# Performance work log

Hardware: AMD Instinct MI355X
Metric: run time of the kernel (lower is better)

## Reference

```python
import jax, jax.numpy as jnp
import numpy as np

B, T, D, H = 512, 128, 128, 2048  # batch, seq_len, input/output dim, hidden dim
W_SCALE = 0.02


def setup_inputs() -> dict:
    key = jax.random.key(0)
    ks = jax.random.split(key, 4)
    return {
        "tgt": jax.random.normal(ks[0], (B, T, D), jnp.float32),
        "W_ih": jax.random.normal(ks[1], (4 * H, D), jnp.float32) * W_SCALE,
        "W_hh": jax.random.normal(ks[2], (4 * H, H), jnp.float32) * W_SCALE,
        "b_ih": jnp.zeros((4 * H,), jnp.float32),
        "b_hh": jnp.zeros((4 * H,), jnp.float32),
        "W_out": jax.random.normal(ks[3], (D, H), jnp.float32) * W_SCALE,
        "b_out": jnp.zeros((D,), jnp.float32),
    }


def reference(tgt, W_ih, W_hh, b_ih, b_hh, W_out, b_out):
    # LSTMDecoder.forward with teacher_forcing_ratio=0.0 (deterministic,
    # tgt: [B, T, D]; first frame tgt[:, 0] seeds the decoder.
    batch, max_len, _ = tgt.shape
    hidden = W_hh.shape[1]
    b = b_ih + b_hh  # fuse the two LSTM biases

    def step(carry, _):
        x, h, c = carry
        # torch nn.LSTM gate order: i, f, g, o
        gates = x @ W_ih.T + h @ W_hh.T + b  # [B, 4H]
        i, f, g, o = jnp.split(gates, 4, axis=-1)
        c = jax.nn.sigmoid(f) * c + jax.nn.sigmoid(i) * jnp.tanh(g)
        h = jax.nn.sigmoid(o) * jnp.tanh(c)
        out = h @ W_out.T + b_out  # [B, D]
        return (out, h, c), out

    h0 = jnp.zeros((batch, hidden), tgt.dtype)
    c0 = jnp.zeros((batch, hidden), tgt.dtype)
    _, outs = jax.lax.scan(step, (tgt[:, 0, :], h0, c0), None, length=max_len)
    return outs.transpose(1, 0, 2)  # [B, T, D]
```

## Files before the change

### kernel.cpp

```cpp
#include <hip/hip_runtime.h>
#include <hip/hip_fp16.h>

typedef _Float16 f16;
typedef __attribute__((ext_vector_type(8))) _Float16 f16x8;
typedef __attribute__((ext_vector_type(16))) float f32x16;

#define GLL(src, dst) __builtin_amdgcn_global_load_lds( \
    (const __attribute__((address_space(1))) void*)(src), \
    (__attribute__((address_space(3))) void*)(dst), 16, 0, 0)

__device__ __forceinline__ void gemm_core(
    const f16* __restrict__ A, int lda,
    const f16* __restrict__ Bm, int ldb,
    int K, int bm0, int nbase, int nstride,
    unsigned char* __restrict__ smem, f32x16 acc[2][2])
{
    const int tid  = threadIdx.x;
    const int wave = tid >> 6;
    const int wr   = wave >> 1;
    const int wc   = wave & 1;
    const int lane = tid & 63;
    const int l31  = lane & 31;
    const int hi   = lane >> 5;

    #pragma unroll
    for (int mt = 0; mt < 2; ++mt)
      #pragma unroll
      for (int nt = 0; nt < 2; ++nt)
        #pragma unroll
        for (int e = 0; e < 16; ++e)
          acc[mt][nt][e] = 0.f;

    const f16* gA[4]; const f16* gB[4];
    int ldA[4], ldB[4];
    #pragma unroll
    for (int p = 0; p < 4; ++p) {
        int s  = p * 256 + tid;
        int r  = s >> 3;
        int cg = (s & 7) ^ (r & 7);
        gA[p] = A + (size_t)(bm0 + r) * lda + cg * 8;
        int brow = nbase + (r >> 5) * nstride + (r & 31);
        gB[p] = Bm + (size_t)brow * ldb + cg * 8;
        ldA[p] = (p * 256 + wave * 64) * 16;
        ldB[p] = 16384 + (p * 256 + wave * 64) * 16;
    }

    int offA[2][4], offB[2][4];
    #pragma unroll
    for (int mt = 0; mt < 2; ++mt) {
        int ra = wr * 64 + mt * 32 + l31;
        #pragma unroll
        for (int kk = 0; kk < 4; ++kk)
            offA[mt][kk] = (ra * 8 + ((kk * 2 + hi) ^ (ra & 7))) * 8;
    }
    #pragma unroll
    for (int nt = 0; nt < 2; ++nt) {
        int rb = wc * 64 + nt * 32 + l31;
        #pragma unroll
        for (int kk = 0; kk < 4; ++kk)
            offB[nt][kk] = 8192 + (rb * 8 + ((kk * 2 + hi) ^ (rb & 7))) * 8;
    }

    auto stage = [&](int buf, int t2) {
        unsigned char* base = smem + buf * 32768;
        const int k0 = t2 * 64;
        #pragma unroll
        for (int p = 0; p < 4; ++p) GLL(gA[p] + k0, base + ldA[p]);
        #pragma unroll
        for (int p = 0; p < 4; ++p) GLL(gB[p] + k0, base + ldB[p]);
    };
    auto rdfr = [&](int buf, f16x8 (&af)[2][4], f16x8 (&bf)[2][4]) {
        const f16* base = (const f16*)(smem + buf * 32768);
        #pragma unroll
        for (int mt = 0; mt < 2; ++mt)
          #pragma unroll
          for (int kk = 0; kk < 4; ++kk)
            af[mt][kk] = *(const f16x8*)(base + offA[mt][kk]);
        #pragma unroll
        for (int nt = 0; nt < 2; ++nt)
          #pragma unroll
          for (int kk = 0; kk < 4; ++kk)
            bf[nt][kk] = *(const f16x8*)(base + offB[nt][kk]);
    };
    auto mm = [&](f16x8 (&af)[2][4], f16x8 (&bf)[2][4]) {
        #pragma unroll
        for (int kk = 0; kk < 4; ++kk)
          #pragma unroll
          for (int mt = 0; mt < 2; ++mt)
            #pragma unroll
            for (int nt = 0; nt < 2; ++nt)
              acc[mt][nt] = __builtin_amdgcn_mfma_f32_32x32x16_f16(
                  af[mt][kk], bf[nt][kk], acc[mt][nt], 0, 0, 0);
    };

    const int niter = K >> 6;
    f16x8 aX[2][4], bX[2][4], aY[2][4], bY[2][4];
    stage(0, 0);
    stage(1, 1);
    asm volatile("s_waitcnt vmcnt(8)" ::: "memory");
    __builtin_amdgcn_s_barrier();
    __builtin_amdgcn_sched_barrier(0);
    rdfr(0, aX, bX);

    for (int t = 0; t < niter; t += 2) {
        asm volatile("s_waitcnt lgkmcnt(0)" ::: "memory");
        __builtin_amdgcn_sched_barrier(0);
        __builtin_amdgcn_s_barrier();
        __builtin_amdgcn_sched_barrier(0);
        if (t + 2 < niter) stage(0, t + 2);
        if (t + 2 < niter) asm volatile("s_waitcnt vmcnt(8)" ::: "memory");
        else               asm volatile("s_waitcnt vmcnt(0)" ::: "memory");
        __builtin_amdgcn_s_barrier();
        __builtin_amdgcn_sched_barrier(0);
        rdfr(1, aY, bY);
        mm(aX, bX);
        asm volatile("s_waitcnt lgkmcnt(0)" ::: "memory");
        __builtin_amdgcn_sched_barrier(0);
        __builtin_amdgcn_s_barrier();
        __builtin_amdgcn_sched_barrier(0);
        if (t + 3 < niter) stage(1, t + 3);
        if (t + 2 < niter) {
            if (t + 3 < niter) asm volatile("s_waitcnt vmcnt(8)" ::: "memory");
            else               asm volatile("s_waitcnt vmcnt(0)" ::: "memory");
            __builtin_amdgcn_s_barrier();
            __builtin_amdgcn_sched_barrier(0);
            rdfr(0, aX, bX);
        }
        mm(aY, bY);
    }
}

__global__ __launch_bounds__(256, 1) void k_step(
    const f16* __restrict__ A, int lda, int K,
    const f16* __restrict__ W, int ldb,
    const float* __restrict__ bias,
    float* __restrict__ Cst,
    f16* __restrict__ Hout)
{
    __shared__ alignas(16) unsigned char smem[65536];
    const int hid0 = blockIdx.x * 32;
    const int bm0  = blockIdx.y * 128;
    f32x16 acc[2][2];
    gemm_core(A, lda, W, ldb, K, bm0, hid0, 2048, smem, acc);

    const int tid = threadIdx.x;
    const int wave = tid >> 6, wr = wave >> 1, wc = wave & 1;
    const int lane = tid & 63, l31 = lane & 31, hi = lane >> 5;
    float* G = (float*)smem;
    #pragma unroll
    for (int mt = 0; mt < 2; ++mt)
      #pragma unroll
      for (int nt = 0; nt < 2; ++nt) {
        const int col = wc * 64 + nt * 32 + l31;
        #pragma unroll
        for (int reg = 0; reg < 16; ++reg) {
          const int row = wr * 64 + mt * 32 + (reg & 3) + 8 * (reg >> 2) + 4 * hi;
          G[row * 128 + col] = acc[mt][nt][reg];
        }
      }
    __syncthreads();
    const int hl  = tid & 31;
    const int r8  = tid >> 5;
    const int hid = hid0 + hl;
    const float bI = bias[hid];
    const float bF = bias[2048 + hid];
    const float bG = bias[4096 + hid];
    const float bO = bias[6144 + hid];
    #pragma unroll
    for (int j = 0; j < 16; ++j) {
        const int row = j * 8 + r8;
        const float* g = G + row * 128;
        float iv = g[hl]      + bI;
        float fv = g[32 + hl] + bF;
        float gv = g[64 + hl] + bG;
        float ov = g[96 + hl] + bO;
        float si = 1.f / (1.f + __expf(-iv));
        float sf = 1.f / (1.f + __expf(-fv));
        float so = 1.f / (1.f + __expf(-ov));
        float tg = tanhf(gv);
        const size_t idx = (size_t)(bm0 + row) * 2048 + hid;
        float c = sf * Cst[idx] + si * tg;
        Cst[idx] = c;
        Hout[idx] = (f16)(so * tanhf(c));
    }
}

__global__ __launch_bounds__(256, 1) void k_out(
    const f16* __restrict__ Hbase,
    const f16* __restrict__ Wout,
    const float* __restrict__ bout,
    float* __restrict__ out, int t0)
{
    __shared__ alignas(16) unsigned char smem[65536];
    const int bm0 = blockIdx.y * 128;
    f32x16 acc[2][2];
    gemm_core(Hbase, 2048, Wout, 2048, 2048, bm0, 0, 32, smem, acc);
    const int tid = threadIdx.x;
    const int wave = tid >> 6, wr = wave >> 1, wc = wave & 1;
    const int lane = tid & 63, l31 = lane & 31, hi = lane >> 5;
    #pragma unroll
    for (int mt = 0; mt < 2; ++mt)
      #pragma unroll
      for (int nt = 0; nt < 2; ++nt) {
        const int d = wc * 64 + nt * 32 + l31;
        const float bo = bout[d];
        #pragma unroll
        for (int reg = 0; reg < 16; ++reg) {
          const int row = wr * 64 + mt * 32 + (reg & 3) + 8 * (reg >> 2) + 4 * hi;
          const int m = bm0 + row;
          const int slot = m >> 9, b = m & 511;
          out[(size_t)b * 16384 + (t0 + slot) * 128 + d] = acc[mt][nt][reg] + bo;
        }
      }
}


__global__ void k_cast(const float* __restrict__ s, f16* __restrict__ d, int n)
{
    int i = blockIdx.x * 256 + threadIdx.x;
    if (i < n) d[i] = (f16)s[i];
}

__global__ void k_x0(const float* __restrict__ tgt, f16* __restrict__ x0)
{
    int i = blockIdx.x * 256 + threadIdx.x;
    int b = i >> 7, d = i & 127;
    x0[i] = (f16)tgt[(size_t)b * 16384 + d];
}

__global__ void k_bias(const float* __restrict__ bih, const float* __restrict__ bhh,
                       const float* __restrict__ Wih, const float* __restrict__ bout,
                       float* __restrict__ b0, float* __restrict__ bp)
{
    int r = blockIdx.x * 256 + threadIdx.x;
    if (r >= 8192) return;
    float s = bih[r] + bhh[r];
    float a = 0.f;
    for (int d = 0; d < 128; ++d) a += Wih[(size_t)r * 128 + d] * bout[d];
    b0[r] = s;
    bp[r] = s + a;
}

__global__ void k_wt(const float* __restrict__ Wout, f16* __restrict__ WoutT)
{
    __shared__ float tile[64][65];
    const int k0 = blockIdx.x * 64;
    const int d0 = blockIdx.y * 64;
    const int tid = threadIdx.x;
    const int c = tid & 63, rr = tid >> 6;
    #pragma unroll
    for (int i = 0; i < 16; ++i) {
        int d = rr + i * 4;
        tile[d][c] = Wout[(size_t)(d0 + d) * 2048 + k0 + c];
    }
    __syncthreads();
    #pragma unroll
    for (int i = 0; i < 16; ++i) {
        int k = rr + i * 4;
        WoutT[(size_t)(k0 + k) * 128 + d0 + c] = (f16)tile[c][k];
    }
}

__global__ __launch_bounds__(256, 1) void k_wcomb2(
    const f16* __restrict__ Wih16, const f16* __restrict__ WoutT,
    const float* __restrict__ Whh, f16* __restrict__ Wc)
{
    __shared__ alignas(16) unsigned char smem[65536];
    const int n0  = blockIdx.x * 128;
    const int bm0 = blockIdx.y * 128;
    f32x16 acc[2][2];
    gemm_core(Wih16, 128, WoutT, 128, 128, bm0, n0, 32, smem, acc);
    const int tid = threadIdx.x;
    const int wave = tid >> 6, wr = wave >> 1, wc = wave & 1;
    const int lane = tid & 63, l31 = lane & 31, hi = lane >> 5;
    #pragma unroll
    for (int mt = 0; mt < 2; ++mt)
      #pragma unroll
      for (int nt = 0; nt < 2; ++nt) {
        const int k = n0 + wc * 64 + nt * 32 + l31;
        #pragma unroll
        for (int reg = 0; reg < 16; ++reg) {
          const int row = wr * 64 + mt * 32 + (reg & 3) + 8 * (reg >> 2) + 4 * hi;
          const size_t r = (size_t)(bm0 + row);
          Wc[r * 2048 + k] = (f16)(acc[mt][nt][reg] + Whh[r * 2048 + k]);
        }
      }
}


extern "C" void kernel_launch(void* const* d_in, const int* in_sizes, int n_in,
                              void* d_out, int out_size, void* d_ws, size_t ws_size,
                              hipStream_t stream)
{
    const float* tgt  = (const float*)d_in[0];
    const float* Wih  = (const float*)d_in[1];
    const float* Whh  = (const float*)d_in[2];
    const float* bih  = (const float*)d_in[3];
    const float* bhh  = (const float*)d_in[4];
    const float* Wout = (const float*)d_in[5];
    const float* bout = (const float*)d_in[6];
    float* out = (float*)d_out;

    char* ws = (char*)d_ws;
    size_t off = 0;
    auto alloc = [&](size_t bytes) -> void* {
        void* p = ws + off;
        off += (bytes + 255) & ~(size_t)255;
        return p;
    };
    f16*   Wc     = (f16*)alloc((size_t)8192 * 2048 * 2);
    f16*   Wih16  = (f16*)alloc((size_t)8192 * 128 * 2);
    f16*   Wout16 = (f16*)alloc((size_t)128 * 2048 * 2);
    f16*   WoutT  = (f16*)alloc((size_t)2048 * 128 * 2);
    f16*   x0     = (f16*)alloc((size_t)512 * 128 * 2);
    float* b0     = (float*)alloc(8192 * 4);
    float* bp     = (float*)alloc(8192 * 4);
    float* Cst    = (float*)alloc((size_t)512 * 2048 * 4);

    const size_t slotsz = (size_t)512 * 2048;
    int depth = 0;
    const int cands[7] = {128, 64, 32, 16, 8, 4, 2};
    for (int i = 0; i < 7; ++i)
        if (off + (size_t)cands[i] * slotsz * 2 <= ws_size) { depth = cands[i]; break; }
    if (depth == 0) return;
    f16* Hbuf = (f16*)alloc((size_t)depth * slotsz * 2);

    hipMemsetAsync(Cst, 0, (size_t)512 * 2048 * 4, stream);
    k_cast<<<dim3(4096), dim3(256), 0, stream>>>(Wih, Wih16, 1048576);
    k_cast<<<dim3(1024), dim3(256), 0, stream>>>(Wout, Wout16, 262144);
    k_wt<<<dim3(32, 2), dim3(256), 0, stream>>>(Wout, WoutT);
    k_x0<<<dim3(256), dim3(256), 0, stream>>>(tgt, x0);
    k_bias<<<dim3(32), dim3(256), 0, stream>>>(bih, bhh, Wih, bout, b0, bp);
    k_wcomb2<<<dim3(16, 64), dim3(256), 0, stream>>>(Wih16, WoutT, Whh, Wc);

    k_step<<<dim3(64, 4), dim3(256), 0, stream>>>(x0, 128, 128, Wih16, 128, b0, Cst, Hbuf);
    for (int s = 1; s < 128; ++s) {
        if ((s % depth) == 0)
            k_out<<<dim3(1, depth * 4), dim3(256), 0, stream>>>(Hbuf, Wout16, bout, out, s - depth);
        k_step<<<dim3(64, 4), dim3(256), 0, stream>>>(
            Hbuf + (size_t)((s - 1) % depth) * slotsz, 2048, 2048, Wc, 2048, bp,
            Cst, Hbuf + (size_t)(s % depth) * slotsz);
    }
    k_out<<<dim3(1, depth * 4), dim3(256), 0, stream>>>(Hbuf, Wout16, bout, out, 128 - depth);
}
```

Baseline: 4.307 ms.

## Split GEMM tile across eight waves with simpler single-buffer-read pipeline

```diff
diff --git a/kernel.cpp b/kernel.cpp
--- a/kernel.cpp
+++ b/kernel.cpp
@@ -13,12 +13,12 @@
     const f16* __restrict__ A, int lda,
     const f16* __restrict__ Bm, int ldb,
     int K, int bm0, int nbase, int nstride,
-    unsigned char* __restrict__ smem, f32x16 acc[2][2])
+    unsigned char* __restrict__ smem, f32x16 acc[2])
 {
     const int tid  = threadIdx.x;
     const int wave = tid >> 6;
-    const int wr   = wave >> 1;
-    const int wc   = wave & 1;
+    const int wr   = wave >> 2;
+    const int wc   = wave & 3;
     const int lane = tid & 63;
     const int l31  = lane & 31;
     const int hi   = lane >> 5;
@@ -26,26 +26,24 @@
     #pragma unroll
     for (int mt = 0; mt < 2; ++mt)
       #pragma unroll
-      for (int nt = 0; nt < 2; ++nt)
-        #pragma unroll
-        for (int e = 0; e < 16; ++e)
-          acc[mt][nt][e] = 0.f;
-
-    const f16* gA[4]; const f16* gB[4];
-    int ldA[4], ldB[4];
-    #pragma unroll
-    for (int p = 0; p < 4; ++p) {
-        int s  = p * 256 + tid;
+      for (int e = 0; e < 16; ++e)
+        acc[mt][e] = 0.f;
+
+    const f16* gA[2]; const f16* gB[2];
+    int ldA[2], ldB[2];
+    #pragma unroll
+    for (int p = 0; p < 2; ++p) {
+        int s  = p * 512 + tid;
         int r  = s >> 3;
         int cg = (s & 7) ^ (r & 7);
         gA[p] = A + (size_t)(bm0 + r) * lda + cg * 8;
         int brow = nbase + (r >> 5) * nstride + (r & 31);
         gB[p] = Bm + (size_t)brow * ldb + cg * 8;
-        ldA[p] = (p * 256 + wave * 64) * 16;
-        ldB[p] = 16384 + (p * 256 + wave * 64) * 16;
-    }
-
-    int offA[2][4], offB[2][4];
+        ldA[p] = (p * 512 + wave * 64) * 16;
+        ldB[p] = 16384 + (p * 512 + wave * 64) * 16;
+    }
+
+    int offA[2][4], offB[4];
     #pragma unroll
     for (int mt = 0; mt < 2; ++mt) {
         int ra = wr * 64 + mt * 32 + l31;
@@ -53,84 +51,55 @@
         for (int kk = 0; kk < 4; ++kk)
             offA[mt][kk] = (ra * 8 + ((kk * 2 + hi) ^ (ra & 7))) * 8;
     }
-    #pragma unroll
-    for (int nt = 0; nt < 2; ++nt) {
-        int rb = wc * 64 + nt * 32 + l31;
+    {
+        int rb = wc * 32 + l31;
         #pragma unroll
         for (int kk = 0; kk < 4; ++kk)
-            offB[nt][kk] = 8192 + (rb * 8 + ((kk * 2 + hi) ^ (rb & 7))) * 8;
+            offB[kk] = 8192 + (rb * 8 + ((kk * 2 + hi) ^ (rb & 7))) * 8;
     }
 
     auto stage = [&](int buf, int t2) {
         unsigned char* base = smem + buf * 32768;
         const int k0 = t2 * 64;
         #pragma unroll
-        for (int p = 0; p < 4; ++p) GLL(gA[p] + k0, base + ldA[p]);
-        #pragma unroll
-        for (int p = 0; p < 4; ++p) GLL(gB[p] + k0, base + ldB[p]);
+        for (int p = 0; p < 2; ++p) GLL(gA[p] + k0, base + ldA[p]);
+        #pragma unroll
+        for (int p = 0; p < 2; ++p) GLL(gB[p] + k0, base + ldB[p]);
     };
-    auto rdfr = [&](int buf, f16x8 (&af)[2][4], f16x8 (&bf)[2][4]) {
-        const f16* base = (const f16*)(smem + buf * 32768);
+
+    const int niter = K >> 6;
+    stage(0, 0);
+    stage(1, 1);
+    for (int t = 0; t < niter; ++t) {
+        if (t + 1 < niter)
+            asm volatile("s_waitcnt vmcnt(4)" ::: "memory");
+        else
+            asm volatile("s_waitcnt vmcnt(0)" ::: "memory");
+        __builtin_amdgcn_s_barrier();
+        const f16* base = (const f16*)(smem + (t & 1) * 32768);
+        f16x8 af[2][4], bf[4];
         #pragma unroll
         for (int mt = 0; mt < 2; ++mt)
           #pragma unroll
           for (int kk = 0; kk < 4; ++kk)
             af[mt][kk] = *(const f16x8*)(base + offA[mt][kk]);
         #pragma unroll
-        for (int nt = 0; nt < 2; ++nt)
-          #pragma unroll
-          for (int kk = 0; kk < 4; ++kk)
-            bf[nt][kk] = *(const f16x8*)(base + offB[nt][kk]);
-    };
-    auto mm = [&](f16x8 (&af)[2][4], f16x8 (&bf)[2][4]) {
+        for (int kk = 0; kk < 4; ++kk)
+            bf[kk] = *(const f16x8*)(base + offB[kk]);
+        asm volatile("s_waitcnt lgkmcnt(0)" ::: "memory");
+        __builtin_amdgcn_sched_barrier(0);
+        __builtin_amdgcn_s_barrier();
+        if (t + 2 < niter) stage(t & 1, t + 2);
         #pragma unroll
         for (int kk = 0; kk < 4; ++kk)
           #pragma unroll
           for (int mt = 0; mt < 2; ++mt)
-            #pragma unroll
-            for (int nt = 0; nt < 2; ++nt)
-              acc[mt][nt] = __builtin_amdgcn_mfma_f32_32x32x16_f16(
-                  af[mt][kk], bf[nt][kk], acc[mt][nt], 0, 0, 0);
-    };
-
-    const int niter = K >> 6;
-    f16x8 aX[2][4], bX[2][4], aY[2][4], bY[2][4];
-    stage(0, 0);
-    stage(1, 1);
-    asm volatile("s_waitcnt vmcnt(8)" ::: "memory");
-    __builtin_amdgcn_s_barrier();
-    __builtin_amdgcn_sched_barrier(0);
-    rdfr(0, aX, bX);
-
-    for (int t = 0; t < niter; t += 2) {
-        asm volatile("s_waitcnt lgkmcnt(0)" ::: "memory");
-        __builtin_amdgcn_sched_barrier(0);
-        __builtin_amdgcn_s_barrier();
-        __builtin_amdgcn_sched_barrier(0);
-        if (t + 2 < niter) stage(0, t + 2);
-        if (t + 2 < niter) asm volatile("s_waitcnt vmcnt(8)" ::: "memory");
-        else               asm volatile("s_waitcnt vmcnt(0)" ::: "memory");
-        __builtin_amdgcn_s_barrier();
-        __builtin_amdgcn_sched_barrier(0);
-        rdfr(1, aY, bY);
-        mm(aX, bX);
-        asm volatile("s_waitcnt lgkmcnt(0)" ::: "memory");
-        __builtin_amdgcn_sched_barrier(0);
-        __builtin_amdgcn_s_barrier();
-        __builtin_amdgcn_sched_barrier(0);
-        if (t + 3 < niter) stage(1, t + 3);
-        if (t + 2 < niter) {
-            if (t + 3 < niter) asm volatile("s_waitcnt vmcnt(8)" ::: "memory");
-            else               asm volatile("s_waitcnt vmcnt(0)" ::: "memory");
-            __builtin_amdgcn_s_barrier();
-            __builtin_amdgcn_sched_barrier(0);
-            rdfr(0, aX, bX);
-        }
-        mm(aY, bY);
-    }
-}
-
-__global__ __launch_bounds__(256, 1) void k_step(
+            acc[mt] = __builtin_amdgcn_mfma_f32_32x32x16_f16(
+                af[mt][kk], bf[kk], acc[mt], 0, 0, 0);
+    }
+}
+
+__global__ __launch_bounds__(512, 2) void k_step(
     const f16* __restrict__ A, int lda, int K,
     const f16* __restrict__ W, int ldb,
     const float* __restrict__ bias,
@@ -140,35 +109,33 @@
     __shared__ alignas(16) unsigned char smem[65536];
     const int hid0 = blockIdx.x * 32;
     const int bm0  = blockIdx.y * 128;
-    f32x16 acc[2][2];
+    f32x16 acc[2];
     gemm_core(A, lda, W, ldb, K, bm0, hid0, 2048, smem, acc);
 
     const int tid = threadIdx.x;
-    const int wave = tid >> 6, wr = wave >> 1, wc = wave & 1;
+    const int wave = tid >> 6, wr = wave >> 2, wc = wave & 3;
     const int lane = tid & 63, l31 = lane & 31, hi = lane >> 5;
     float* G = (float*)smem;
     #pragma unroll
-    for (int mt = 0; mt < 2; ++mt)
-      #pragma unroll
-      for (int nt = 0; nt < 2; ++nt) {
-        const int col = wc * 64 + nt * 32 + l31;
+    for (int mt = 0; mt < 2; ++mt) {
+        const int col = wc * 32 + l31;
         #pragma unroll
         for (int reg = 0; reg < 16; ++reg) {
-          const int row = wr * 64 + mt * 32 + (reg & 3) + 8 * (reg >> 2) + 4 * hi;
-          G[row * 128 + col] = acc[mt][nt][reg];
+            const int row = wr * 64 + mt * 32 + (reg & 3) + 8 * (reg >> 2) + 4 * hi;
+            G[row * 128 + col] = acc[mt][reg];
         }
-      }
+    }
     __syncthreads();
     const int hl  = tid & 31;
-    const int r8  = tid >> 5;
+    const int r16 = tid >> 5;
     const int hid = hid0 + hl;
     const float bI = bias[hid];
     const float bF = bias[2048 + hid];
     const float bG = bias[4096 + hid];
     const float bO = bias[6144 + hid];
     #pragma unroll
-    for (int j = 0; j < 16; ++j) {
-        const int row = j * 8 + r8;
+    for (int j = 0; j < 8; ++j) {
+        const int row = j * 16 + r16;
         const float* g = G + row * 128;
         float iv = g[hl]      + bI;
         float fv = g[32 + hl] + bF;
@@ -185,7 +152,7 @@
     }
 }
 
-__global__ __launch_bounds__(256, 1) void k_out(
+__global__ __launch_bounds__(512, 2) void k_out(
     const f16* __restrict__ Hbase,
     const f16* __restrict__ Wout,
     const float* __restrict__ bout,
@@ -193,25 +160,23 @@
 {
     __shared__ alignas(16) unsigned char smem[65536];
     const int bm0 = blockIdx.y * 128;
-    f32x16 acc[2][2];
+    f32x16 acc[2];
     gemm_core(Hbase, 2048, Wout, 2048, 2048, bm0, 0, 32, smem, acc);
     const int tid = threadIdx.x;
-    const int wave = tid >> 6, wr = wave >> 1, wc = wave & 1;
+    const int wave = tid >> 6, wr = wave >> 2, wc = wave & 3;
     const int lane = tid & 63, l31 = lane & 31, hi = lane >> 5;
-    #pragma unroll
-    for (int mt = 0; mt < 2; ++mt)
-      #pragma unroll
-      for (int nt = 0; nt < 2; ++nt) {
-        const int d = wc * 64 + nt * 32 + l31;
-        const float bo = bout[d];
+    const int d = wc * 32 + l31;
+    const float bo = bout[d];
+    #pragma unroll
+    for (int mt = 0; mt < 2; ++mt) {
         #pragma unroll
         for (int reg = 0; reg < 16; ++reg) {
-          const int row = wr * 64 + mt * 32 + (reg & 3) + 8 * (reg >> 2) + 4 * hi;
-          const int m = bm0 + row;
-          const int slot = m >> 9, b = m & 511;
-          out[(size_t)b * 16384 + (t0 + slot) * 128 + d] = acc[mt][nt][reg] + bo;
+            const int row = wr * 64 + mt * 32 + (reg & 3) + 8 * (reg >> 2) + 4 * hi;
+            const int m = bm0 + row;
+            const int slot = m >> 9, b = m & 511;
+            out[(size_t)b * 16384 + (t0 + slot) * 128 + d] = acc[mt][reg] + bo;
         }
-      }
+    }
 }
 
 
@@ -261,30 +226,28 @@
     }
 }
 
-__global__ __launch_bounds__(256, 1) void k_wcomb2(
+__global__ __launch_bounds__(512, 2) void k_wcomb2(
     const f16* __restrict__ Wih16, const f16* __restrict__ WoutT,
     const float* __restrict__ Whh, f16* __restrict__ Wc)
 {
     __shared__ alignas(16) unsigned char smem[65536];
     const int n0  = blockIdx.x * 128;
     const int bm0 = blockIdx.y * 128;
-    f32x16 acc[2][2];
+    f32x16 acc[2];
     gemm_core(Wih16, 128, WoutT, 128, 128, bm0, n0, 32, smem, acc);
     const int tid = threadIdx.x;
-    const int wave = tid >> 6, wr = wave >> 1, wc = wave & 1;
+    const int wave = tid >> 6, wr = wave >> 2, wc = wave & 3;
     const int lane = tid & 63, l31 = lane & 31, hi = lane >> 5;
-    #pragma unroll
-    for (int mt = 0; mt < 2; ++mt)
-      #pragma unroll
-      for (int nt = 0; nt < 2; ++nt) {
-        const int k = n0 + wc * 64 + nt * 32 + l31;
+    const int k = n0 + wc * 32 + l31;
+    #pragma unroll
+    for (int mt = 0; mt < 2; ++mt) {
         #pragma unroll
         for (int reg = 0; reg < 16; ++reg) {
-          const int row = wr * 64 + mt * 32 + (reg & 3) + 8 * (reg >> 2) + 4 * hi;
-          const size_t r = (size_t)(bm0 + row);
-          Wc[r * 2048 + k] = (f16)(acc[mt][nt][reg] + Whh[r * 2048 + k]);
+            const int row = wr * 64 + mt * 32 + (reg & 3) + 8 * (reg >> 2) + 4 * hi;
+            const size_t r = (size_t)(bm0 + row);
+            Wc[r * 2048 + k] = (f16)(acc[mt][reg] + Whh[r * 2048 + k]);
         }
-      }
+    }
 }
 
 
@@ -331,15 +294,15 @@
     k_wt<<<dim3(32, 2), dim3(256), 0, stream>>>(Wout, WoutT);
     k_x0<<<dim3(256), dim3(256), 0, stream>>>(tgt, x0);
     k_bias<<<dim3(32), dim3(256), 0, stream>>>(bih, bhh, Wih, bout, b0, bp);
-    k_wcomb2<<<dim3(16, 64), dim3(256), 0, stream>>>(Wih16, WoutT, Whh, Wc);
-
-    k_step<<<dim3(64, 4), dim3(256), 0, stream>>>(x0, 128, 128, Wih16, 128, b0, Cst, Hbuf);
+    k_wcomb2<<<dim3(16, 64), dim3(512), 0, stream>>>(Wih16, WoutT, Whh, Wc);
+
+    k_step<<<dim3(64, 4), dim3(512), 0, stream>>>(x0, 128, 128, Wih16, 128, b0, Cst, Hbuf);
     for (int s = 1; s < 128; ++s) {
         if ((s % depth) == 0)
-            k_out<<<dim3(1, depth * 4), dim3(256), 0, stream>>>(Hbuf, Wout16, bout, out, s - depth);
-        k_step<<<dim3(64, 4), dim3(256), 0, stream>>>(
+            k_out<<<dim3(1, depth * 4), dim3(512), 0, stream>>>(Hbuf, Wout16, bout, out, s - depth);
+        k_step<<<dim3(64, 4), dim3(512), 0, stream>>>(
             Hbuf + (size_t)((s - 1) % depth) * slotsz, 2048, 2048, Wc, 2048, bp,
             Cst, Hbuf + (size_t)(s % depth) * slotsz);
     }
-    k_out<<<dim3(1, depth * 4), dim3(256), 0, stream>>>(Hbuf, Wout16, bout, out, 128 - depth);
-}
+    k_out<<<dim3(1, depth * 4), dim3(512), 0, stream>>>(Hbuf, Wout16, bout, out, 128 - depth);
+}
```

After: 4.556 ms. +5.8%, slower.

## Pre-tile operands into MFMA fragment layout and load A directly to registers

Applied to the files above, without the earlier changes.

```diff
diff --git a/kernel.cpp b/kernel.cpp
--- a/kernel.cpp
+++ b/kernel.cpp
@@ -9,20 +9,16 @@
     (const __attribute__((address_space(1))) void*)(src), \
     (__attribute__((address_space(3))) void*)(dst), 16, 0, 0)
 
-__device__ __forceinline__ void gemm_core(
-    const f16* __restrict__ A, int lda,
-    const f16* __restrict__ Bm, int ldb,
-    int K, int bm0, int nbase, int nstride,
-    unsigned char* __restrict__ smem, f32x16 acc[2][2])
-{
-    const int tid  = threadIdx.x;
-    const int wave = tid >> 6;
-    const int wr   = wave >> 1;
-    const int wc   = wave & 1;
-    const int lane = tid & 63;
-    const int l31  = lane & 31;
-    const int hi   = lane >> 5;
-
+__device__ __forceinline__ size_t foff(int r, int k, int nkb) {
+    return ((size_t)((r >> 5) * nkb + (k >> 4)) << 9)
+         + (size_t)(((((k >> 3) & 1)) << 8) + ((r & 31) << 3) + (k & 7));
+}
+
+__device__ __forceinline__ void rgemm(
+    const f16* __restrict__ pA0, const f16* __restrict__ pA1,
+    const f16* __restrict__ pB0, const f16* __restrict__ pB1,
+    f16* sB, int wv, int lane, int n, f32x16 acc[2][2])
+{
     #pragma unroll
     for (int mt = 0; mt < 2; ++mt)
       #pragma unroll
@@ -31,201 +27,241 @@
         for (int e = 0; e < 16; ++e)
           acc[mt][nt][e] = 0.f;
 
-    const f16* gA[4]; const f16* gB[4];
-    int ldA[4], ldB[4];
-    #pragma unroll
-    for (int p = 0; p < 4; ++p) {
-        int s  = p * 256 + tid;
-        int r  = s >> 3;
-        int cg = (s & 7) ^ (r & 7);
-        gA[p] = A + (size_t)(bm0 + r) * lda + cg * 8;
-        int brow = nbase + (r >> 5) * nstride + (r & 31);
-        gB[p] = Bm + (size_t)brow * ldb + cg * 8;
-        ldA[p] = (p * 256 + wave * 64) * 16;
-        ldB[p] = 16384 + (p * 256 + wave * 64) * 16;
-    }
-
-    int offA[2][4], offB[2][4];
-    #pragma unroll
-    for (int mt = 0; mt < 2; ++mt) {
-        int ra = wr * 64 + mt * 32 + l31;
-        #pragma unroll
-        for (int kk = 0; kk < 4; ++kk)
-            offA[mt][kk] = (ra * 8 + ((kk * 2 + hi) ^ (ra & 7))) * 8;
-    }
-    #pragma unroll
-    for (int nt = 0; nt < 2; ++nt) {
-        int rb = wc * 64 + nt * 32 + l31;
-        #pragma unroll
-        for (int kk = 0; kk < 4; ++kk)
-            offB[nt][kk] = 8192 + (rb * 8 + ((kk * 2 + hi) ^ (rb & 7))) * 8;
-    }
-
-    auto stage = [&](int buf, int t2) {
-        unsigned char* base = smem + buf * 32768;
-        const int k0 = t2 * 64;
-        #pragma unroll
-        for (int p = 0; p < 4; ++p) GLL(gA[p] + k0, base + ldA[p]);
-        #pragma unroll
-        for (int p = 0; p < 4; ++p) GLL(gB[p] + k0, base + ldB[p]);
+    f16x8 X[2][2], Y[2][2];
+    auto LA = [&](f16x8 (&R)[2][2], int t) {
+        size_t o = (size_t)t * 1024;
+        R[0][0] = *(const f16x8*)(pA0 + o);
+        R[0][1] = *(const f16x8*)(pA0 + o + 512);
+        R[1][0] = *(const f16x8*)(pA1 + o);
+        R[1][1] = *(const f16x8*)(pA1 + o + 512);
     };
-    auto rdfr = [&](int buf, f16x8 (&af)[2][4], f16x8 (&bf)[2][4]) {
-        const f16* base = (const f16*)(smem + buf * 32768);
-        #pragma unroll
-        for (int mt = 0; mt < 2; ++mt)
-          #pragma unroll
-          for (int kk = 0; kk < 4; ++kk)
-            af[mt][kk] = *(const f16x8*)(base + offA[mt][kk]);
+    auto BG = [&](int buf, int t) {
+        size_t o = (size_t)t * 1024;
+        GLL(pB0 + o, sB + buf * 2048 + wv * 512);
+        GLL(pB1 + o, sB + buf * 2048 + 1024 + wv * 512);
+    };
+    auto STEP = [&](f16x8 (&R)[2][2], int buf, int t, bool last) {
+        if (last) asm volatile("s_waitcnt vmcnt(0)" ::: "memory");
+        else      asm volatile("s_waitcnt vmcnt(6)" ::: "memory");
+        __builtin_amdgcn_sched_barrier(0);
+        __builtin_amdgcn_s_barrier();
+        __builtin_amdgcn_sched_barrier(0);
+        f16x8 bf[2][2];
+        const f16* bb = sB + buf * 2048 + lane * 8;
         #pragma unroll
         for (int nt = 0; nt < 2; ++nt)
           #pragma unroll
-          for (int kk = 0; kk < 4; ++kk)
-            bf[nt][kk] = *(const f16x8*)(base + offB[nt][kk]);
-    };
-    auto mm = [&](f16x8 (&af)[2][4], f16x8 (&bf)[2][4]) {
-        #pragma unroll
-        for (int kk = 0; kk < 4; ++kk)
+          for (int kk = 0; kk < 2; ++kk)
+            bf[nt][kk] = *(const f16x8*)(bb + nt * 1024 + kk * 512);
+        asm volatile("s_waitcnt lgkmcnt(0)" ::: "memory");
+        __builtin_amdgcn_sched_barrier(0);
+        __builtin_amdgcn_s_barrier();
+        __builtin_amdgcn_sched_barrier(0);
+        if (t + 2 < n) BG(buf, t + 2);
+        __builtin_amdgcn_s_setprio(1);
+        #pragma unroll
+        for (int kk = 0; kk < 2; ++kk)
           #pragma unroll
           for (int mt = 0; mt < 2; ++mt)
             #pragma unroll
             for (int nt = 0; nt < 2; ++nt)
               acc[mt][nt] = __builtin_amdgcn_mfma_f32_32x32x16_f16(
-                  af[mt][kk], bf[nt][kk], acc[mt][nt], 0, 0, 0);
+                  R[mt][kk], bf[nt][kk], acc[mt][nt], 0, 0, 0);
+        __builtin_amdgcn_s_setprio(0);
+        if (t + 2 < n) LA(R, t + 2);
     };
 
-    const int niter = K >> 6;
-    f16x8 aX[2][4], bX[2][4], aY[2][4], bY[2][4];
-    stage(0, 0);
-    stage(1, 1);
-    asm volatile("s_waitcnt vmcnt(8)" ::: "memory");
-    __builtin_amdgcn_s_barrier();
     __builtin_amdgcn_sched_barrier(0);
-    rdfr(0, aX, bX);
-
-    for (int t = 0; t < niter; t += 2) {
-        asm volatile("s_waitcnt lgkmcnt(0)" ::: "memory");
-        __builtin_amdgcn_sched_barrier(0);
-        __builtin_amdgcn_s_barrier();
-        __builtin_amdgcn_sched_barrier(0);
-        if (t + 2 < niter) stage(0, t + 2);
-        if (t + 2 < niter) asm volatile("s_waitcnt vmcnt(8)" ::: "memory");
-        else               asm volatile("s_waitcnt vmcnt(0)" ::: "memory");
-        __builtin_amdgcn_s_barrier();
-        __builtin_amdgcn_sched_barrier(0);
-        rdfr(1, aY, bY);
-        mm(aX, bX);
-        asm volatile("s_waitcnt lgkmcnt(0)" ::: "memory");
-        __builtin_amdgcn_sched_barrier(0);
-        __builtin_amdgcn_s_barrier();
-        __builtin_amdgcn_sched_barrier(0);
-        if (t + 3 < niter) stage(1, t + 3);
-        if (t + 2 < niter) {
-            if (t + 3 < niter) asm volatile("s_waitcnt vmcnt(8)" ::: "memory");
-            else               asm volatile("s_waitcnt vmcnt(0)" ::: "memory");
-            __builtin_amdgcn_s_barrier();
-            __builtin_amdgcn_sched_barrier(0);
-            rdfr(0, aX, bX);
-        }
-        mm(aY, bY);
-    }
-}
-
-__global__ __launch_bounds__(256, 1) void k_step(
-    const f16* __restrict__ A, int lda, int K,
-    const f16* __restrict__ W, int ldb,
+    BG(0, 0); LA(X, 0);
+    __builtin_amdgcn_sched_barrier(0);
+    BG(1, 1); LA(Y, 1);
+    __builtin_amdgcn_sched_barrier(0);
+    for (int t = 0; t < n; t += 2) {
+        STEP(X, 0, t, false);
+        STEP(Y, 1, t + 1, t + 2 >= n);
+    }
+}
+
+#define PICKV(ii) ((ii) == 0 ? w0[e] : (ii) == 1 ? w1[e] : (ii) == 2 ? w2[e] : w3[e])
+
+__global__ __launch_bounds__(128) void k_step(
+    const f16* __restrict__ Af, int nkb,
+    const f16* __restrict__ Bf,
     const float* __restrict__ bias,
     float* __restrict__ Cst,
     f16* __restrict__ Hout)
 {
-    __shared__ alignas(16) unsigned char smem[65536];
-    const int hid0 = blockIdx.x * 32;
-    const int bm0  = blockIdx.y * 128;
+    __shared__ alignas(16) f16 sB[4096];
+    const int P = blockIdx.x;
+    const int L = (P & 7) * ((int)gridDim.x >> 3) + (P >> 3);
+    const int cg = L >> 2, rg = L & 3;
+    const int tid = threadIdx.x;
+    const int wv = tid >> 6, lane = tid & 63;
+    const int l31 = lane & 31, hi = lane >> 5;
+    const int mb = rg * 4 + wv * 2;
+    const int nb = cg * 2;
+    const f16* pA0 = Af + ((size_t)mb * nkb) * 512 + lane * 8;
+    const f16* pA1 = pA0 + (size_t)nkb * 512;
+    const f16* pB0 = Bf + ((size_t)nb * nkb + wv) * 512 + (size_t)lane * 8;
+    const f16* pB1 = pB0 + (size_t)nkb * 512;
     f32x16 acc[2][2];
-    gemm_core(A, lda, W, ldb, K, bm0, hid0, 2048, smem, acc);
-
+    rgemm(pA0, pA1, pB0, pB1, sB, wv, lane, nkb >> 1, acc);
+
+    const int g = l31 & 3;
+    #pragma unroll
+    for (int nt = 0; nt < 2; ++nt) {
+        const int hid = cg * 16 + nt * 8 + (l31 >> 2);
+        const float bown = bias[(g << 11) + hid];
+        #pragma unroll
+        for (int mt = 0; mt < 2; ++mt) {
+            float w0[16], w1[16], w2[16], w3[16];
+            #pragma unroll
+            for (int e = 0; e < 16; ++e) {
+                float x = acc[mt][nt][e] + bown;
+                float xx = (g == 2) ? 2.f * x : x;
+                float s = 1.f / (1.f + __expf(-xx));
+                w0[e] = (g == 2) ? 2.f * s - 1.f : s;
+            }
+            #pragma unroll
+            for (int e = 0; e < 16; ++e) {
+                w1[e] = __shfl_xor(w0[e], 1);
+                w2[e] = __shfl_xor(w0[e], 2);
+                w3[e] = __shfl_xor(w0[e], 3);
+            }
+            const int rowb = rg * 128 + wv * 64 + mt * 32 + 4 * hi;
+            #pragma unroll
+            for (int eg = 0; eg < 4; ++eg) {
+                if (g == eg) {
+                    #pragma unroll
+                    for (int q = 0; q < 4; ++q) {
+                        const int e = eg * 4 + q;
+                        const float iv = PICKV(eg ^ 0);
+                        const float fv = PICKV(eg ^ 1);
+                        const float gv = PICKV(eg ^ 2);
+                        const float ov = PICKV(eg ^ 3);
+                        const int row = rowb + q + 8 * eg;
+                        const size_t cidx = (size_t)row * 2048 + hid;
+                        const float c = fv * Cst[cidx] + iv * gv;
+                        Cst[cidx] = c;
+                        Hout[foff(row, hid, 128)] = (f16)(ov * tanhf(c));
+                    }
+                }
+            }
+        }
+    }
+}
+
+__global__ __launch_bounds__(128) void k_out(
+    const f16* __restrict__ Hbase, const f16* __restrict__ Bf,
+    const float* __restrict__ bout, float* __restrict__ out,
+    int t0, int rgshift)
+{
+    __shared__ alignas(16) f16 sB[4096];
+    const int P = blockIdx.x;
+    const int L = (P & 7) * ((int)gridDim.x >> 3) + (P >> 3);
+    const int cg = L >> rgshift;
+    const int rg = L & ((1 << rgshift) - 1);
     const int tid = threadIdx.x;
-    const int wave = tid >> 6, wr = wave >> 1, wc = wave & 1;
-    const int lane = tid & 63, l31 = lane & 31, hi = lane >> 5;
-    float* G = (float*)smem;
+    const int wv = tid >> 6, lane = tid & 63;
+    const int l31 = lane & 31, hi = lane >> 5;
+    const int mbg = rg * 4 + wv * 2;
+    const int slot = mbg >> 4, mloc = mbg & 15;
+    const f16* pA0 = Hbase + (size_t)slot * 1048576
+                   + ((size_t)mloc * 128) * 512 + lane * 8;
+    const f16* pA1 = pA0 + 128 * 512;
+    const int nb = cg * 2;
+    const f16* pB0 = Bf + ((size_t)nb * 128 + wv) * 512 + (size_t)lane * 8;
+    const f16* pB1 = pB0 + (size_t)128 * 512;
+    f32x16 acc[2][2];
+    rgemm(pA0, pA1, pB0, pB1, sB, wv, lane, 64, acc);
+
     #pragma unroll
-    for (int mt = 0; mt < 2; ++mt)
-      #pragma unroll
-      for (int nt = 0; nt < 2; ++nt) {
-        const int col = wc * 64 + nt * 32 + l31;
-        #pragma unroll
-        for (int reg = 0; reg < 16; ++reg) {
-          const int row = wr * 64 + mt * 32 + (reg & 3) + 8 * (reg >> 2) + 4 * hi;
-          G[row * 128 + col] = acc[mt][nt][reg];
-        }
-      }
-    __syncthreads();
-    const int hl  = tid & 31;
-    const int r8  = tid >> 5;
-    const int hid = hid0 + hl;
-    const float bI = bias[hid];
-    const float bF = bias[2048 + hid];
-    const float bG = bias[4096 + hid];
-    const float bO = bias[6144 + hid];
+    for (int nt = 0; nt < 2; ++nt) {
+        const int d = cg * 64 + nt * 32 + l31;
+        const float bo = bout[d];
+        #pragma unroll
+        for (int mt = 0; mt < 2; ++mt)
+          #pragma unroll
+          for (int e = 0; e < 16; ++e) {
+            const int m = rg * 128 + wv * 64 + mt * 32
+                        + (e & 3) + 8 * (e >> 2) + 4 * hi;
+            out[(size_t)(m & 511) * 16384 + (size_t)(t0 + (m >> 9)) * 128 + d]
+                = acc[mt][nt][e] + bo;
+          }
+    }
+}
+
+__global__ __launch_bounds__(128) void k_wcomb(
+    const f16* __restrict__ Af,
+    const f16* __restrict__ Bf,
+    const float* __restrict__ Whh, f16* __restrict__ Wf)
+{
+    __shared__ alignas(16) f16 sB[4096];
+    const int P = blockIdx.x;
+    const int L = (P & 7) * ((int)gridDim.x >> 3) + (P >> 3);
+    const int cg = L >> 6, rg = L & 63;
+    const int tid = threadIdx.x;
+    const int wv = tid >> 6, lane = tid & 63;
+    const int l31 = lane & 31, hi = lane >> 5;
+    const int mb = rg * 4 + wv * 2, nb = cg * 2;
+    const f16* pA0 = Af + ((size_t)mb * 8) * 512 + lane * 8;
+    const f16* pA1 = pA0 + 8 * 512;
+    const f16* pB0 = Bf + ((size_t)nb * 8 + wv) * 512 + (size_t)lane * 8;
+    const f16* pB1 = pB0 + 8 * 512;
+    f32x16 acc[2][2];
+    rgemm(pA0, pA1, pB0, pB1, sB, wv, lane, 4, acc);
+
     #pragma unroll
-    for (int j = 0; j < 16; ++j) {
-        const int row = j * 8 + r8;
-        const float* g = G + row * 128;
-        float iv = g[hl]      + bI;
-        float fv = g[32 + hl] + bF;
-        float gv = g[64 + hl] + bG;
-        float ov = g[96 + hl] + bO;
-        float si = 1.f / (1.f + __expf(-iv));
-        float sf = 1.f / (1.f + __expf(-fv));
-        float so = 1.f / (1.f + __expf(-ov));
-        float tg = tanhf(gv);
-        const size_t idx = (size_t)(bm0 + row) * 2048 + hid;
-        float c = sf * Cst[idx] + si * tg;
-        Cst[idx] = c;
-        Hout[idx] = (f16)(so * tanhf(c));
-    }
-}
-
-__global__ __launch_bounds__(256, 1) void k_out(
-    const f16* __restrict__ Hbase,
-    const f16* __restrict__ Wout,
-    const float* __restrict__ bout,
-    float* __restrict__ out, int t0)
-{
-    __shared__ alignas(16) unsigned char smem[65536];
-    const int bm0 = blockIdx.y * 128;
-    f32x16 acc[2][2];
-    gemm_core(Hbase, 2048, Wout, 2048, 2048, bm0, 0, 32, smem, acc);
-    const int tid = threadIdx.x;
-    const int wave = tid >> 6, wr = wave >> 1, wc = wave & 1;
-    const int lane = tid & 63, l31 = lane & 31, hi = lane >> 5;
-    #pragma unroll
-    for (int mt = 0; mt < 2; ++mt)
-      #pragma unroll
-      for (int nt = 0; nt < 2; ++nt) {
-        const int d = wc * 64 + nt * 32 + l31;
-        const float bo = bout[d];
-        #pragma unroll
-        for (int reg = 0; reg < 16; ++reg) {
-          const int row = wr * 64 + mt * 32 + (reg & 3) + 8 * (reg >> 2) + 4 * hi;
-          const int m = bm0 + row;
-          const int slot = m >> 9, b = m & 511;
-          out[(size_t)b * 16384 + (t0 + slot) * 128 + d] = acc[mt][nt][reg] + bo;
-        }
-      }
-}
-
-
-__global__ void k_cast(const float* __restrict__ s, f16* __restrict__ d, int n)
-{
-    int i = blockIdx.x * 256 + threadIdx.x;
-    if (i < n) d[i] = (f16)s[i];
-}
-
-__global__ void k_x0(const float* __restrict__ tgt, f16* __restrict__ x0)
-{
-    int i = blockIdx.x * 256 + threadIdx.x;
-    int b = i >> 7, d = i & 127;
-    x0[i] = (f16)tgt[(size_t)b * 16384 + d];
+    for (int nt = 0; nt < 2; ++nt) {
+        const int kc = cg * 64 + nt * 32 + l31;
+        #pragma unroll
+        for (int mt = 0; mt < 2; ++mt)
+          #pragma unroll
+          for (int e = 0; e < 16; ++e) {
+            const int r = rg * 128 + wv * 64 + mt * 32
+                        + (e & 3) + 8 * (e >> 2) + 4 * hi;
+            const float v = acc[mt][nt][e] + Whh[(size_t)r * 2048 + kc];
+            const int rho = ((r & 2047) << 2) | (r >> 11);
+            Wf[foff(rho, kc, 128)] = (f16)v;
+          }
+    }
+}
+
+
+__global__ void k_x0f(const float* __restrict__ tgt, f16* __restrict__ x0f)
+{
+    int i = blockIdx.x * 256 + threadIdx.x;
+    int b = i >> 7, k = i & 127;
+    x0f[foff(b, k, 8)] = (f16)tgt[(size_t)b * 16384 + k];
+}
+
+__global__ void k_wihf(const float* __restrict__ Wih, f16* __restrict__ Wihf)
+{
+    int i = blockIdx.x * 256 + threadIdx.x;
+    int rho = i >> 7, k = i & 127;
+    int gate = rho & 3, hid = rho >> 2;
+    Wihf[foff(rho, k, 8)] = (f16)Wih[((size_t)gate * 2048 + hid) * 128 + k];
+}
+
+__global__ void k_wihaf(const float* __restrict__ Wih, f16* __restrict__ Wihaf)
+{
+    int i = blockIdx.x * 256 + threadIdx.x;
+    int r = i >> 7, k = i & 127;
+    Wihaf[foff(r, k, 8)] = (f16)Wih[(size_t)r * 128 + k];
+}
+
+__global__ void k_woutTf(const float* __restrict__ Wout, f16* __restrict__ WoutTf)
+{
+    int i = blockIdx.x * 256 + threadIdx.x;
+    int d = i >> 11, n = i & 2047;
+    WoutTf[foff(n, d, 8)] = (f16)Wout[(size_t)d * 2048 + n];
+}
+
+__global__ void k_woutf(const float* __restrict__ Wout, f16* __restrict__ Woutf)
+{
+    int i = blockIdx.x * 256 + threadIdx.x;
+    int d = i >> 11, k = i & 2047;
+    Woutf[foff(d, k, 128)] = (f16)Wout[(size_t)d * 2048 + k];
 }
 
 __global__ void k_bias(const float* __restrict__ bih, const float* __restrict__ bhh,
@@ -239,52 +275,6 @@
     for (int d = 0; d < 128; ++d) a += Wih[(size_t)r * 128 + d] * bout[d];
     b0[r] = s;
     bp[r] = s + a;
-}
-
-__global__ void k_wt(const float* __restrict__ Wout, f16* __restrict__ WoutT)
-{
-    __shared__ float tile[64][65];
-    const int k0 = blockIdx.x * 64;
-    const int d0 = blockIdx.y * 64;
-    const int tid = threadIdx.x;
-    const int c = tid & 63, rr = tid >> 6;
-    #pragma unroll
-    for (int i = 0; i < 16; ++i) {
-        int d = rr + i * 4;
-        tile[d][c] = Wout[(size_t)(d0 + d) * 2048 + k0 + c];
-    }
-    __syncthreads();
-    #pragma unroll
-    for (int i = 0; i < 16; ++i) {
-        int k = rr + i * 4;
-        WoutT[(size_t)(k0 + k) * 128 + d0 + c] = (f16)tile[c][k];
-    }
-}
-
-__global__ __launch_bounds__(256, 1) void k_wcomb2(
-    const f16* __restrict__ Wih16, const f16* __restrict__ WoutT,
-    const float* __restrict__ Whh, f16* __restrict__ Wc)
-{
-    __shared__ alignas(16) unsigned char smem[65536];
-    const int n0  = blockIdx.x * 128;
-    const int bm0 = blockIdx.y * 128;
-    f32x16 acc[2][2];
-    gemm_core(Wih16, 128, WoutT, 128, 128, bm0, n0, 32, smem, acc);
-    const int tid = threadIdx.x;
-    const int wave = tid >> 6, wr = wave >> 1, wc = wave & 1;
-    const int lane = tid & 63, l31 = lane & 31, hi = lane >> 5;
-    #pragma unroll
-    for (int mt = 0; mt < 2; ++mt)
-      #pragma unroll
-      for (int nt = 0; nt < 2; ++nt) {
-        const int k = n0 + wc * 64 + nt * 32 + l31;
-        #pragma unroll
-        for (int reg = 0; reg < 16; ++reg) {
-          const int row = wr * 64 + mt * 32 + (reg & 3) + 8 * (reg >> 2) + 4 * hi;
-          const size_t r = (size_t)(bm0 + row);
-          Wc[r * 2048 + k] = (f16)(acc[mt][nt][reg] + Whh[r * 2048 + k]);
-        }
-      }
 }
 
 
@@ -308,11 +298,12 @@
         off += (bytes + 255) & ~(size_t)255;
         return p;
     };
-    f16*   Wc     = (f16*)alloc((size_t)8192 * 2048 * 2);
-    f16*   Wih16  = (f16*)alloc((size_t)8192 * 128 * 2);
-    f16*   Wout16 = (f16*)alloc((size_t)128 * 2048 * 2);
-    f16*   WoutT  = (f16*)alloc((size_t)2048 * 128 * 2);
-    f16*   x0     = (f16*)alloc((size_t)512 * 128 * 2);
+    f16*   Wf     = (f16*)alloc((size_t)8192 * 2048 * 2);
+    f16*   Wihf   = (f16*)alloc((size_t)8192 * 128 * 2);
+    f16*   Wihaf  = (f16*)alloc((size_t)8192 * 128 * 2);
+    f16*   WoutTf = (f16*)alloc((size_t)2048 * 128 * 2);
+    f16*   Woutf  = (f16*)alloc((size_t)128 * 2048 * 2);
+    f16*   x0f    = (f16*)alloc((size_t)512 * 128 * 2);
     float* b0     = (float*)alloc(8192 * 4);
     float* bp     = (float*)alloc(8192 * 4);
     float* Cst    = (float*)alloc((size_t)512 * 2048 * 4);
@@ -324,22 +315,26 @@
         if (off + (size_t)cands[i] * slotsz * 2 <= ws_size) { depth = cands[i]; break; }
     if (depth == 0) return;
     f16* Hbuf = (f16*)alloc((size_t)depth * slotsz * 2);
+    const int rgshift = __builtin_ctz((unsigned)(depth * 4));
 
     hipMemsetAsync(Cst, 0, (size_t)512 * 2048 * 4, stream);
-    k_cast<<<dim3(4096), dim3(256), 0, stream>>>(Wih, Wih16, 1048576);
-    k_cast<<<dim3(1024), dim3(256), 0, stream>>>(Wout, Wout16, 262144);
-    k_wt<<<dim3(32, 2), dim3(256), 0, stream>>>(Wout, WoutT);
-    k_x0<<<dim3(256), dim3(256), 0, stream>>>(tgt, x0);
-    k_bias<<<dim3(32), dim3(256), 0, stream>>>(bih, bhh, Wih, bout, b0, bp);
-    k_wcomb2<<<dim3(16, 64), dim3(256), 0, stream>>>(Wih16, WoutT, Whh, Wc);
-
-    k_step<<<dim3(64, 4), dim3(256), 0, stream>>>(x0, 128, 128, Wih16, 128, b0, Cst, Hbuf);
+    k_x0f   <<<dim3(256),  dim3(256), 0, stream>>>(tgt, x0f);
+    k_wihf  <<<dim3(4096), dim3(256), 0, stream>>>(Wih, Wihf);
+    k_wihaf <<<dim3(4096), dim3(256), 0, stream>>>(Wih, Wihaf);
+    k_woutTf<<<dim3(1024), dim3(256), 0, stream>>>(Wout, WoutTf);
+    k_woutf <<<dim3(1024), dim3(256), 0, stream>>>(Wout, Woutf);
+    k_bias  <<<dim3(32),   dim3(256), 0, stream>>>(bih, bhh, Wih, bout, b0, bp);
+    k_wcomb <<<dim3(2048), dim3(128), 0, stream>>>(Wihaf, WoutTf, Whh, Wf);
+
+    k_step<<<dim3(512), dim3(128), 0, stream>>>(x0f, 8, Wihf, b0, Cst, Hbuf);
     for (int s = 1; s < 128; ++s) {
         if ((s % depth) == 0)
-            k_out<<<dim3(1, depth * 4), dim3(256), 0, stream>>>(Hbuf, Wout16, bout, out, s - depth);
-        k_step<<<dim3(64, 4), dim3(256), 0, stream>>>(
-            Hbuf + (size_t)((s - 1) % depth) * slotsz, 2048, 2048, Wc, 2048, bp,
+            k_out<<<dim3(8 * depth), dim3(128), 0, stream>>>(
+                Hbuf, Woutf, bout, out, s - depth, rgshift);
+        k_step<<<dim3(512), dim3(128), 0, stream>>>(
+            Hbuf + (size_t)((s - 1) % depth) * slotsz, 128, Wf, bp,
             Cst, Hbuf + (size_t)(s % depth) * slotsz);
     }
-    k_out<<<dim3(1, depth * 4), dim3(256), 0, stream>>>(Hbuf, Wout16, bout, out, 128 - depth);
-}
+    k_out<<<dim3(8 * depth), dim3(128), 0, stream>>>(
+        Hbuf, Woutf, bout, out, 128 - depth, rgshift);
+}
```

Measured after the change: 6.953 ms. 61.4% more time.
